# Kernel tuning notes

Hardware: AMD Instinct MI355X
Metric: run time of the kernel (lower is better)

Reference implementation:

```python
import jax, jax.numpy as jnp
import numpy as np

HASH_BINS = 100000
EMB = 64
B = 262144


def _glorot(key, shape):
    fan_in, fan_out = shape[0], shape[-1]
    std = np.sqrt(2.0 / (fan_in + fan_out)).astype(np.float32)
    return jax.random.normal(key, shape, dtype=jnp.float32) * std


def setup_inputs() -> dict:
    key = jax.random.key(0)
    ks = jax.random.split(key, 16)
    return {
        "user_idx": jax.random.randint(ks[0], (B,), 0, HASH_BINS, dtype=jnp.int32),
        "item_idx": jax.random.randint(ks[1], (B,), 0, HASH_BINS, dtype=jnp.int32),
        "user_emb": jax.random.normal(ks[2], (HASH_BINS, EMB), dtype=jnp.float32) * 0.05,
        "item_emb": jax.random.normal(ks[3], (HASH_BINS, EMB), dtype=jnp.float32) * 0.05,
        "lin_w": jax.random.normal(ks[4], (2 * HASH_BINS,), dtype=jnp.float32) * 0.01,
        "lin_b": jnp.zeros((1,), jnp.float32),
        "cross_k": _glorot(ks[5], (2 * EMB, 2 * EMB)),
        "W1": _glorot(ks[6], (2 * EMB, 200)), "b1": jnp.zeros((200,), jnp.float32),
        "W2": _glorot(ks[7], (200, 256)),     "b2": jnp.zeros((256,), jnp.float32),
        "W3": _glorot(ks[8], (256, 200)),     "b3": jnp.zeros((200,), jnp.float32),
        "W4": _glorot(ks[9], (200, 128)),     "b4": jnp.zeros((128,), jnp.float32),
        "W5": _glorot(ks[10], (128, 1)),      "b5": jnp.zeros((1,), jnp.float32),
    }


def reference(user_idx, item_idx, user_emb, item_emb, lin_w, lin_b, cross_k,
              W1, b1, W2, b2, W3, b3, W4, b4, W5, b5):
    # Embedding lookups (flattened + concatenated): [B, 2*EMB]
    emb = jnp.concatenate([user_emb[user_idx], item_emb[item_idx]], axis=1)

    # FM linear term. CategoryEncoding(multi-hot over 2*HASH_BINS) -> Dense(1)
    # is exactly a gather-sum of the dense kernel rows (one user + one item token).
    linear = (lin_w[user_idx] + lin_w[HASH_BINS + item_idx] + lin_b)[:, None]  # [B,1]

    # FM cross term: 0.5 * mean((xK)^2 - x^2 K^2, axis=1)
    xk = emb @ cross_k                      # [B, 128]
    x2k2 = (emb * emb) @ (cross_k * cross_k)
    cross = 0.5 * jnp.mean(xk * xk - x2k2, axis=1, keepdims=True)  # [B,1]

    # Deep MLP (inference: no dropout)
    h = jax.nn.relu(emb @ W1 + b1)
    h = jax.nn.relu(h @ W2 + b2)
    h = jax.nn.relu(h @ W3 + b3)
    h = jax.nn.relu(h @ W4 + b4)
    dnn = h @ W5 + b5                       # [B,1]

    return jax.nn.sigmoid(linear + cross + dnn)
```

## Files before the change

kernel.cpp:

```cpp
#include <hip/hip_runtime.h>

#define HASH_BINS 100000
#define EMBD 64
#define BATCH 262144
#define BM 64
#define SA 264
#define SB 232

typedef __attribute__((ext_vector_type(8))) short short8;
typedef __attribute__((ext_vector_type(4))) float floatx4;
typedef __attribute__((ext_vector_type(4))) unsigned short ushortx4;

static __device__ __forceinline__ unsigned short f2bf(float f) {
  unsigned u = __builtin_bit_cast(unsigned, f);
  u += 0x7fff + ((u >> 16) & 1);
  return (unsigned short)(u >> 16);
}
static __device__ __forceinline__ float bf2f(unsigned short b) {
  return __builtin_bit_cast(float, ((unsigned)b) << 16);
}

__global__ void dfm_prep(const float* __restrict__ K, const float* __restrict__ W1,
                         const float* __restrict__ W2, const float* __restrict__ W3,
                         const float* __restrict__ W4,
                         float* __restrict__ S, unsigned short* __restrict__ Kt,
                         unsigned short* __restrict__ W1t, unsigned short* __restrict__ W2t,
                         unsigned short* __restrict__ W3t, unsigned short* __restrict__ W4t)
{
  int idx = blockIdx.x * 256 + threadIdx.x;
  if (idx < 128) {
    float s = 0.f;
    for (int j = 0; j < 128; j++) { float v = K[idx * 128 + j]; s += v * v; }
    S[idx] = s;
  }
  int i = idx;
  if (i < 16384) {
    int k = i >> 7, n = i & 127;
    Kt[n * 128 + k] = f2bf(K[i]);
  } else if ((i -= 16384) < 25600) {
    int k = i / 200, n = i - k * 200;
    W1t[n * 128 + k] = f2bf(W1[i]);
  } else if ((i -= 25600) < 3072) {
    int n = 200 + (i >> 7), k = i & 127;
    W1t[n * 128 + k] = 0;
  } else if ((i -= 3072) < 51200) {
    int k = i >> 8, n = i & 255;
    W2t[n * 224 + k] = f2bf(W2[i]);
  } else if ((i -= 51200) < 6144) {
    int n = i / 24, k = 200 + (i - n * 24);
    W2t[n * 224 + k] = 0;
  } else if ((i -= 6144) < 51200) {
    int k = i / 200, n = i - k * 200;
    W3t[n * 256 + k] = f2bf(W3[i]);
  } else if ((i -= 51200) < 6144) {
    int n = 200 + (i >> 8), k = i & 255;
    W3t[n * 256 + k] = 0;
  } else if ((i -= 6144) < 25600) {
    int k = i >> 7, n = i & 127;
    W4t[n * 224 + k] = f2bf(W4[i]);
  } else if ((i -= 25600) < 3072) {
    int n = i / 24, k = 200 + (i - n * 24);
    W4t[n * 224 + k] = 0;
  }
}

template <int KP, int CH>
static __device__ __forceinline__ void mfma_pass(const unsigned short* __restrict__ wt,
                                                 int rowOff, const unsigned short* actIn,
                                                 int sin, int m, int qd, floatx4* acc)
{
#pragma unroll
  for (int i = 0; i < CH * 4; i++) acc[i] = {0.f, 0.f, 0.f, 0.f};
#pragma unroll
  for (int ks = 0; ks < KP / 32; ks++) {
    short8 a[4];
#pragma unroll
    for (int rt = 0; rt < 4; rt++)
      a[rt] = *(const short8*)&actIn[(rt * 16 + m) * sin + ks * 32 + qd * 8];
#pragma unroll
    for (int n = 0; n < CH; n++) {
      short8 b = *(const short8*)&wt[(rowOff + n * 16 + m) * KP + ks * 32 + qd * 8];
#pragma unroll
      for (int rt = 0; rt < 4; rt++)
        acc[n * 4 + rt] = __builtin_amdgcn_mfma_f32_16x16x32_bf16(a[rt], b, acc[n * 4 + rt], 0, 0, 0);
    }
  }
}

template <int CH>
static __device__ __forceinline__ void epilogue_relu(const float* __restrict__ bias,
                                                     int colBase, int nreal,
                                                     unsigned short* actOut, int sout,
                                                     int m, int qd, const floatx4* acc)
{
#pragma unroll
  for (int n = 0; n < CH; n++) {
    int col = colBase + n * 16 + m;
    float bv = (col < nreal) ? bias[col] : 0.f;
#pragma unroll
    for (int rt = 0; rt < 4; rt++)
#pragma unroll
      for (int i = 0; i < 4; i++) {
        float v = fmaxf(acc[n * 4 + rt][i] + bv, 0.f);
        actOut[(rt * 16 + qd * 4 + i) * sout + col] = f2bf(v);
      }
  }
}

__global__ __launch_bounds__(512)
void dfm_main(const int* __restrict__ uidx, const int* __restrict__ iidx,
              const float* __restrict__ uemb, const float* __restrict__ iemb,
              const float* __restrict__ linw, const float* __restrict__ linb,
              const float* __restrict__ b1, const float* __restrict__ b2,
              const float* __restrict__ b3, const float* __restrict__ b4,
              const float* __restrict__ W5, const float* __restrict__ b5,
              const float* __restrict__ S, const unsigned short* __restrict__ Wc,
              const unsigned short* __restrict__ W2t, const unsigned short* __restrict__ W3t,
              const unsigned short* __restrict__ W4t,
              float* __restrict__ out)
{
  __shared__ unsigned short actA[BM * SA];
  __shared__ unsigned short actB[BM * SB];
  __shared__ float crosspart[4][BM];
  __shared__ float part[BM][8];
  __shared__ float linrow[BM];

  const int t = threadIdx.x;
  const int lane = t & 63, wave = t >> 6;
  const int m = lane & 15, qd = lane >> 4;
  const int r = t >> 3, c = t & 7;

  {
    int g = blockIdx.x * BM + r;
    int u = uidx[g], it = iidx[g];
    const float* up = uemb + (long)u * EMBD + c * 8;
    const float* ip = iemb + (long)it * EMBD + c * 8;
    float qp = 0.f;
#pragma unroll
    for (int j = 0; j < 8; j += 4) {
      float4 f = *(const float4*)(up + j);
      int col = c * 8 + j;
      float4 sv = *(const float4*)(S + col);
      ushortx4 h = {f2bf(f.x), f2bf(f.y), f2bf(f.z), f2bf(f.w)};
      *(ushortx4*)&actA[r * SA + col] = h;
      qp += f.x * f.x * sv.x + f.y * f.y * sv.y + f.z * f.z * sv.z + f.w * f.w * sv.w;
    }
#pragma unroll
    for (int j = 0; j < 8; j += 4) {
      float4 f = *(const float4*)(ip + j);
      int col = 64 + c * 8 + j;
      float4 sv = *(const float4*)(S + col);
      ushortx4 h = {f2bf(f.x), f2bf(f.y), f2bf(f.z), f2bf(f.w)};
      *(ushortx4*)&actA[r * SA + col] = h;
      qp += f.x * f.x * sv.x + f.y * f.y * sv.y + f.z * f.z * sv.z + f.w * f.w * sv.w;
    }
    part[r][c] = qp;
    if (c == 0) linrow[r] = linw[u] + linw[HASH_BINS + it] + linb[0];
  }
  __syncthreads();

  if (wave < 4) {
    floatx4 acc[8];
    mfma_pass<128, 2>(Wc, (2 * wave) * 16, actA, SA, m, qd, acc);
    float s[4][4];
#pragma unroll
    for (int rt = 0; rt < 4; rt++)
#pragma unroll
      for (int i = 0; i < 4; i++)
        s[rt][i] = acc[rt][i] * acc[rt][i] + acc[4 + rt][i] * acc[4 + rt][i];
#pragma unroll
    for (int mask = 1; mask < 16; mask <<= 1)
#pragma unroll
      for (int rt = 0; rt < 4; rt++)
#pragma unroll
        for (int i = 0; i < 4; i++)
          s[rt][i] += __shfl_xor(s[rt][i], mask, 64);
    if (m == 0)
#pragma unroll
      for (int rt = 0; rt < 4; rt++)
#pragma unroll
        for (int i = 0; i < 4; i++)
          crosspart[wave][rt * 16 + qd * 4 + i] = s[rt][i];
    floatx4 acc2[4];
    mfma_pass<128, 1>(Wc, 128 + wave * 16, actA, SA, m, qd, acc2);
    epilogue_relu<1>(b1, wave * 16, 200, actB, SB, m, qd, acc2);
  } else if (wave < 6) {
    int s0 = 4 + (wave - 4) * 3;
    floatx4 acc[12];
    mfma_pass<128, 3>(Wc, 128 + s0 * 16, actA, SA, m, qd, acc);
    epilogue_relu<3>(b1, s0 * 16, 200, actB, SB, m, qd, acc);
  } else {
    int s0 = 10 + (wave - 6) * 2;
    floatx4 acc[8];
    mfma_pass<128, 2>(Wc, 128 + s0 * 16, actA, SA, m, qd, acc);
    epilogue_relu<2>(b1, s0 * 16, 200, actB, SB, m, qd, acc);
  }
  __syncthreads();

  {
    floatx4 acc[8];
    mfma_pass<224, 2>(W2t, wave * 2 * 16, actB, SB, m, qd, acc);
    epilogue_relu<2>(b2, wave * 2 * 16, 256, actA, SA, m, qd, acc);
  }
  __syncthreads();

  if (wave < 6) {
    floatx4 acc[8];
    mfma_pass<256, 2>(W3t, wave * 2 * 16, actA, SA, m, qd, acc);
    epilogue_relu<2>(b3, wave * 2 * 16, 200, actB, SB, m, qd, acc);
  } else {
    int s0 = 12 + (wave - 6);
    floatx4 acc[4];
    mfma_pass<256, 1>(W3t, s0 * 16, actA, SA, m, qd, acc);
    epilogue_relu<1>(b3, s0 * 16, 200, actB, SB, m, qd, acc);
  }
  __syncthreads();

  {
    floatx4 acc[4];
    mfma_pass<224, 1>(W4t, wave * 16, actB, SB, m, qd, acc);
    epilogue_relu<1>(b4, wave * 16, 128, actA, SA, m, qd, acc);
  }
  __syncthreads();

  {
    float qp = part[r][c];
    float d = 0.f;
    const unsigned short* ap = &actA[r * SA + c * 16];
#pragma unroll
    for (int j = 0; j < 2; j++) {
      short8 h = *(const short8*)(ap + j * 8);
      float4 w0 = *(const float4*)(W5 + c * 16 + j * 8);
      float4 w1 = *(const float4*)(W5 + c * 16 + j * 8 + 4);
      d += bf2f((unsigned short)h[0]) * w0.x + bf2f((unsigned short)h[1]) * w0.y +
           bf2f((unsigned short)h[2]) * w0.z + bf2f((unsigned short)h[3]) * w0.w +
           bf2f((unsigned short)h[4]) * w1.x + bf2f((unsigned short)h[5]) * w1.y +
           bf2f((unsigned short)h[6]) * w1.z + bf2f((unsigned short)h[7]) * w1.w;
    }
    const float inv = 0.5f / 128.f;
    part[r][c] = d - inv * qp;
    __syncthreads();
    if (c == 0) {
      float xk2 = crosspart[0][r] + crosspart[1][r] + crosspart[2][r] + crosspart[3][r];
      float dnn = part[r][0] + part[r][1] + part[r][2] + part[r][3] +
                  part[r][4] + part[r][5] + part[r][6] + part[r][7];
      float logit = linrow[r] + inv * xk2 + dnn + b5[0];
      out[blockIdx.x * BM + r] = 1.f / (1.f + expf(-logit));
    }
  }
}

extern "C" void kernel_launch(void* const* d_in, const int* in_sizes, int n_in,
                              void* d_out, int out_size, void* d_ws, size_t ws_size,
                              hipStream_t stream)
{
  const int*   uidx = (const int*)d_in[0];
  const int*   iidx = (const int*)d_in[1];
  const float* uemb = (const float*)d_in[2];
  const float* iemb = (const float*)d_in[3];
  const float* linw = (const float*)d_in[4];
  const float* linb = (const float*)d_in[5];
  const float* K    = (const float*)d_in[6];
  const float* W1   = (const float*)d_in[7];
  const float* b1   = (const float*)d_in[8];
  const float* W2   = (const float*)d_in[9];
  const float* b2   = (const float*)d_in[10];
  const float* W3   = (const float*)d_in[11];
  const float* b3   = (const float*)d_in[12];
  const float* W4   = (const float*)d_in[13];
  const float* b4   = (const float*)d_in[14];
  const float* W5   = (const float*)d_in[15];
  const float* b5   = (const float*)d_in[16];

  char* w = (char*)d_ws;
  float* S = (float*)w;
  unsigned short* Kt  = (unsigned short*)(w + 512);
  unsigned short* W1t = (unsigned short*)(w + 33280);
  unsigned short* W2t = (unsigned short*)(w + 90624);
  unsigned short* W3t = (unsigned short*)(w + 205312);
  unsigned short* W4t = (unsigned short*)(w + 320000);
  float* out = (float*)d_out;

  dfm_prep<<<736, 256, 0, stream>>>(K, W1, W2, W3, W4, S, Kt, W1t, W2t, W3t, W4t);
  dfm_main<<<BATCH / BM, 512, 0, stream>>>(uidx, iidx, uemb, iemb, linw, linb,
                                           b1, b2, b3, b4, W5, b5,
                                           S, Kt, W2t, W3t, W4t, out);
}
```

Measured before the change: 289.3 us.

## Retile MFMA work as 2x4 wave grid with swapped operands and vectorized epilogue

Waves are now arranged as 2 row groups by 4 column groups, so each wave computes 32 rows by a wider slice of output columns. This replaces the old layout where each wave covered all 64 rows with a narrow column slice. The MFMA operands are swapped (weights as A, activations as B), which transposes the accumulator layout. That lets the epilogue write 4 contiguous bf16 values and load the bias as a float4. The cross-term reduction needs fewer shuffles, but per-wave weight-load traffic grows and the first layer's work is split unevenly across waves.

```diff
diff --git a/kernel.cpp b/kernel.cpp
--- a/kernel.cpp
+++ b/kernel.cpp
@@ -66,23 +66,21 @@
 
 template <int KP, int CH>
 static __device__ __forceinline__ void mfma_pass(const unsigned short* __restrict__ wt,
-                                                 int rowOff, const unsigned short* actIn,
-                                                 int sin, int m, int qd, floatx4* acc)
-{
-#pragma unroll
-  for (int i = 0; i < CH * 4; i++) acc[i] = {0.f, 0.f, 0.f, 0.f};
+                                                 int tileRow0, const unsigned short* actIn,
+                                                 int sin, int rbase, int m, int qd,
+                                                 floatx4* acc)
+{
+#pragma unroll
+  for (int i = 0; i < CH * 2; i++) acc[i] = {0.f, 0.f, 0.f, 0.f};
 #pragma unroll
   for (int ks = 0; ks < KP / 32; ks++) {
-    short8 a[4];
-#pragma unroll
-    for (int rt = 0; rt < 4; rt++)
-      a[rt] = *(const short8*)&actIn[(rt * 16 + m) * sin + ks * 32 + qd * 8];
+    short8 a0 = *(const short8*)&actIn[(rbase + m) * sin + ks * 32 + qd * 8];
+    short8 a1 = *(const short8*)&actIn[(rbase + 16 + m) * sin + ks * 32 + qd * 8];
 #pragma unroll
     for (int n = 0; n < CH; n++) {
-      short8 b = *(const short8*)&wt[(rowOff + n * 16 + m) * KP + ks * 32 + qd * 8];
-#pragma unroll
-      for (int rt = 0; rt < 4; rt++)
-        acc[n * 4 + rt] = __builtin_amdgcn_mfma_f32_16x16x32_bf16(a[rt], b, acc[n * 4 + rt], 0, 0, 0);
+      short8 w = *(const short8*)&wt[(tileRow0 + n * 16 + m) * KP + ks * 32 + qd * 8];
+      acc[n * 2 + 0] = __builtin_amdgcn_mfma_f32_16x16x32_bf16(w, a0, acc[n * 2 + 0], 0, 0, 0);
+      acc[n * 2 + 1] = __builtin_amdgcn_mfma_f32_16x16x32_bf16(w, a1, acc[n * 2 + 1], 0, 0, 0);
     }
   }
 }
@@ -91,19 +89,25 @@
 static __device__ __forceinline__ void epilogue_relu(const float* __restrict__ bias,
                                                      int colBase, int nreal,
                                                      unsigned short* actOut, int sout,
-                                                     int m, int qd, const floatx4* acc)
+                                                     int rbase, int m, int qd,
+                                                     const floatx4* acc)
 {
 #pragma unroll
   for (int n = 0; n < CH; n++) {
-    int col = colBase + n * 16 + m;
-    float bv = (col < nreal) ? bias[col] : 0.f;
-#pragma unroll
-    for (int rt = 0; rt < 4; rt++)
-#pragma unroll
-      for (int i = 0; i < 4; i++) {
-        float v = fmaxf(acc[n * 4 + rt][i] + bv, 0.f);
-        actOut[(rt * 16 + qd * 4 + i) * sout + col] = f2bf(v);
-      }
+    int col = colBase + n * 16 + qd * 4;
+    float b0 = 0.f, b1 = 0.f, b2 = 0.f, b3 = 0.f;
+    if (col < nreal) {
+      float4 q = *(const float4*)(bias + col);
+      b0 = q.x; b1 = q.y; b2 = q.z; b3 = q.w;
+    }
+#pragma unroll
+    for (int rt = 0; rt < 2; rt++) {
+      ushortx4 h = { f2bf(fmaxf(acc[n * 2 + rt][0] + b0, 0.f)),
+                     f2bf(fmaxf(acc[n * 2 + rt][1] + b1, 0.f)),
+                     f2bf(fmaxf(acc[n * 2 + rt][2] + b2, 0.f)),
+                     f2bf(fmaxf(acc[n * 2 + rt][3] + b3, 0.f)) };
+      *(ushortx4*)&actOut[(rbase + rt * 16 + m) * sout + col] = h;
+    }
   }
 }
 
@@ -121,13 +125,15 @@
 {
   __shared__ unsigned short actA[BM * SA];
   __shared__ unsigned short actB[BM * SB];
-  __shared__ float crosspart[4][BM];
+  __shared__ float crosspart[2][BM];
   __shared__ float part[BM][8];
   __shared__ float linrow[BM];
 
   const int t = threadIdx.x;
   const int lane = t & 63, wave = t >> 6;
   const int m = lane & 15, qd = lane >> 4;
+  const int rg = wave >> 2, cg = wave & 3;
+  const int rbase = rg * 32;
   const int r = t >> 3, c = t & 7;
 
   {
@@ -159,67 +165,69 @@
   }
   __syncthreads();
 
-  if (wave < 4) {
+  if (cg == 0) {
+    floatx4 acc[12];
+    mfma_pass<128, 6>(Wc, 0, actA, SA, rbase, m, qd, acc);
+    float s0 = 0.f, s1 = 0.f;
+#pragma unroll
+    for (int n = 0; n < 6; n++)
+#pragma unroll
+      for (int i = 0; i < 4; i++) {
+        s0 += acc[n * 2 + 0][i] * acc[n * 2 + 0][i];
+        s1 += acc[n * 2 + 1][i] * acc[n * 2 + 1][i];
+      }
+    s0 += __shfl_xor(s0, 16, 64); s0 += __shfl_xor(s0, 32, 64);
+    s1 += __shfl_xor(s1, 16, 64); s1 += __shfl_xor(s1, 32, 64);
+    if (qd == 0) { crosspart[0][rbase + m] = s0; crosspart[0][rbase + 16 + m] = s1; }
+  } else if (cg == 1) {
+    floatx4 acc[12];
+    mfma_pass<128, 6>(Wc, 96, actA, SA, rbase, m, qd, acc);
+    float s0 = 0.f, s1 = 0.f;
+#pragma unroll
+    for (int n = 0; n < 2; n++)
+#pragma unroll
+      for (int i = 0; i < 4; i++) {
+        s0 += acc[n * 2 + 0][i] * acc[n * 2 + 0][i];
+        s1 += acc[n * 2 + 1][i] * acc[n * 2 + 1][i];
+      }
+    s0 += __shfl_xor(s0, 16, 64); s0 += __shfl_xor(s0, 32, 64);
+    s1 += __shfl_xor(s1, 16, 64); s1 += __shfl_xor(s1, 32, 64);
+    if (qd == 0) { crosspart[1][rbase + m] = s0; crosspart[1][rbase + 16 + m] = s1; }
+    epilogue_relu<4>(b1, 0, 200, actB, SB, rbase, m, qd, acc + 4);
+  } else if (cg == 2) {
+    floatx4 acc[10];
+    mfma_pass<128, 5>(Wc, 192, actA, SA, rbase, m, qd, acc);
+    epilogue_relu<5>(b1, 64, 200, actB, SB, rbase, m, qd, acc);
+  } else {
+    floatx4 acc[10];
+    mfma_pass<128, 5>(Wc, 272, actA, SA, rbase, m, qd, acc);
+    epilogue_relu<5>(b1, 144, 200, actB, SB, rbase, m, qd, acc);
+  }
+  __syncthreads();
+
+  {
     floatx4 acc[8];
-    mfma_pass<128, 2>(Wc, (2 * wave) * 16, actA, SA, m, qd, acc);
-    float s[4][4];
-#pragma unroll
-    for (int rt = 0; rt < 4; rt++)
-#pragma unroll
-      for (int i = 0; i < 4; i++)
-        s[rt][i] = acc[rt][i] * acc[rt][i] + acc[4 + rt][i] * acc[4 + rt][i];
-#pragma unroll
-    for (int mask = 1; mask < 16; mask <<= 1)
-#pragma unroll
-      for (int rt = 0; rt < 4; rt++)
-#pragma unroll
-        for (int i = 0; i < 4; i++)
-          s[rt][i] += __shfl_xor(s[rt][i], mask, 64);
-    if (m == 0)
-#pragma unroll
-      for (int rt = 0; rt < 4; rt++)
-#pragma unroll
-        for (int i = 0; i < 4; i++)
-          crosspart[wave][rt * 16 + qd * 4 + i] = s[rt][i];
-    floatx4 acc2[4];
-    mfma_pass<128, 1>(Wc, 128 + wave * 16, actA, SA, m, qd, acc2);
-    epilogue_relu<1>(b1, wave * 16, 200, actB, SB, m, qd, acc2);
-  } else if (wave < 6) {
-    int s0 = 4 + (wave - 4) * 3;
-    floatx4 acc[12];
-    mfma_pass<128, 3>(Wc, 128 + s0 * 16, actA, SA, m, qd, acc);
-    epilogue_relu<3>(b1, s0 * 16, 200, actB, SB, m, qd, acc);
+    mfma_pass<224, 4>(W2t, cg * 64, actB, SB, rbase, m, qd, acc);
+    epilogue_relu<4>(b2, cg * 64, 256, actA, SA, rbase, m, qd, acc);
+  }
+  __syncthreads();
+
+  if (cg < 2) {
+    floatx4 acc[8];
+    mfma_pass<256, 4>(W3t, cg * 64, actA, SA, rbase, m, qd, acc);
+    epilogue_relu<4>(b3, cg * 64, 200, actB, SB, rbase, m, qd, acc);
   } else {
-    int s0 = 10 + (wave - 6) * 2;
-    floatx4 acc[8];
-    mfma_pass<128, 2>(Wc, 128 + s0 * 16, actA, SA, m, qd, acc);
-    epilogue_relu<2>(b1, s0 * 16, 200, actB, SB, m, qd, acc);
-  }
-  __syncthreads();
-
-  {
-    floatx4 acc[8];
-    mfma_pass<224, 2>(W2t, wave * 2 * 16, actB, SB, m, qd, acc);
-    epilogue_relu<2>(b2, wave * 2 * 16, 256, actA, SA, m, qd, acc);
-  }
-  __syncthreads();
-
-  if (wave < 6) {
-    floatx4 acc[8];
-    mfma_pass<256, 2>(W3t, wave * 2 * 16, actA, SA, m, qd, acc);
-    epilogue_relu<2>(b3, wave * 2 * 16, 200, actB, SB, m, qd, acc);
-  } else {
-    int s0 = 12 + (wave - 6);
+    floatx4 acc[6];
+    int s0 = 128 + (cg - 2) * 48;
+    mfma_pass<256, 3>(W3t, s0, actA, SA, rbase, m, qd, acc);
+    epilogue_relu<3>(b3, s0, 200, actB, SB, rbase, m, qd, acc);
+  }
+  __syncthreads();
+
+  {
     floatx4 acc[4];
-    mfma_pass<256, 1>(W3t, s0 * 16, actA, SA, m, qd, acc);
-    epilogue_relu<1>(b3, s0 * 16, 200, actB, SB, m, qd, acc);
-  }
-  __syncthreads();
-
-  {
-    floatx4 acc[4];
-    mfma_pass<224, 1>(W4t, wave * 16, actB, SB, m, qd, acc);
-    epilogue_relu<1>(b4, wave * 16, 128, actA, SA, m, qd, acc);
+    mfma_pass<224, 2>(W4t, cg * 32, actB, SB, rbase, m, qd, acc);
+    epilogue_relu<2>(b4, cg * 32, 128, actA, SA, rbase, m, qd, acc);
   }
   __syncthreads();
 
@@ -241,7 +249,7 @@
     part[r][c] = d - inv * qp;
     __syncthreads();
     if (c == 0) {
-      float xk2 = crosspart[0][r] + crosspart[1][r] + crosspart[2][r] + crosspart[3][r];
+      float xk2 = crosspart[0][r] + crosspart[1][r];
       float dnn = part[r][0] + part[r][1] + part[r][2] + part[r][3] +
                   part[r][4] + part[r][5] + part[r][6] + part[r][7];
       float logit = linrow[r] + inv * xk2 + dnn + b5[0];
```

Result: slower. 414.5 us (+43.3%).
